# Optimization experiments

Hardware: AMD Instinct MI355X
Metric: run time of the kernel (lower is better)

Reference implementation:

```python
import jax, jax.numpy as jnp
import numpy as np

B, S = 512, 2048
E_DIM, P_DIM, C_DIM, H_DIM = 64, 32, 64, 64
NEG = jnp.float32(-2**32 + 1)  # padding value used by the torch module


def setup_inputs() -> dict:
    key = jax.random.key(0)
    ks = jax.random.split(key, 9)
    return {
        "seq_items": jax.random.normal(ks[0], (B, S, E_DIM), dtype=jnp.float32),
        "seq_pos": jax.random.normal(ks[1], (B, S, P_DIM), dtype=jnp.float32),
        "target_item": jax.random.normal(ks[2], (B, C_DIM), dtype=jnp.float32),
        "Wp": jax.random.normal(ks[3], (P_DIM, H_DIM), dtype=jnp.float32) * (2.0 / (P_DIM + H_DIM)) ** 0.5,
        "We": jax.random.normal(ks[4], (E_DIM, H_DIM), dtype=jnp.float32) * (2.0 / (E_DIM + H_DIM)) ** 0.5,
        "Wc": jax.random.normal(ks[5], (C_DIM, H_DIM), dtype=jnp.float32) * (2.0 / (C_DIM + H_DIM)) ** 0.5,
        "b": jnp.zeros((H_DIM,), dtype=jnp.float32),
        "z": jnp.ones((H_DIM,), dtype=jnp.float32),
        "seq_len": jax.random.randint(ks[6], (B,), 0, S, dtype=jnp.int32),
    }


def reference(seq_items, seq_pos, target_item, Wp, We, Wc, b, z, seq_len):
    # Projections: [B,h] and [B,S,h]
    out_c = target_item @ Wc                      # [B, h]
    out_e = jnp.einsum("bse,eh->bsh", seq_items, We)
    out_p = jnp.einsum("bsp,ph->bsh", seq_pos, Wp)
    # Additive attention score: [B, S]
    a = jnp.sum(jnp.tanh(out_c[:, None, :] + out_p + out_e + b) * z, axis=-1)
    # seq_len mask
    mask = jnp.arange(seq_items.shape[1])[None, :] < seq_len[:, None]  # [B, S]
    score = jax.nn.softmax(jnp.where(mask, a, NEG), axis=1)            # [B, S]
    # u = score @ e -> [B, 1, e_dim]  (intended unsqueeze(1) matmul)
    u = jnp.einsum("bs,bse->be", score, seq_items)[:, None, :]
    # r = sum of masked raw scores -> [B, 1]
    r = jnp.sum(jnp.where(mask, a, 0.0), axis=1, keepdims=True)
    return (u, r)
```

## Files before the change

### kernel.cpp

```cpp
#include <hip/hip_runtime.h>
#include <math.h>

#define B_ 512
#define S_ 2048
#define E_DIM 64
#define P_DIM 32
#define H_DIM 64

typedef short s16x8 __attribute__((ext_vector_type(8)));
typedef float f32x4 __attribute__((ext_vector_type(4)));

__device__ __forceinline__ float wave_reduce_sum(float v) {
#pragma unroll
  for (int m = 32; m >= 1; m >>= 1) v += __shfl_xor(v, m, 64);
  return v;
}

__device__ __forceinline__ float wave_reduce_max(float v) {
#pragma unroll
  for (int m = 32; m >= 1; m >>= 1) v = fmaxf(v, __shfl_xor(v, m, 64));
  return v;
}

__device__ __forceinline__ float tanh_fast(float x) {
  float e = __expf(2.0f * x);
  return 1.0f - 2.0f * __builtin_amdgcn_rcpf(e + 1.0f);
}

__device__ __forceinline__ short bf16b(float x) {
  union { float f; unsigned u; } a;
  a.f = x;
  unsigned r = (a.u + 0x7FFFu + ((a.u >> 16) & 1u)) >> 16;
  return (short)r;
}

__global__ __launch_bounds__(256) void scores_mfma_kernel(
    const float* __restrict__ seq_items, const float* __restrict__ seq_pos,
    const float* __restrict__ target_item, const float* __restrict__ Wp,
    const float* __restrict__ We, const float* __restrict__ Wc,
    const float* __restrict__ bias, const float* __restrict__ z,
    const int* __restrict__ seq_len, float* __restrict__ a_out) {
  const int blk = blockIdx.x;
  const int b = blk >> 4;
  const int s0 = (blk & 15) << 7;
  const int L = seq_len[b];
  if (s0 >= L) return;

  __shared__ s16x8 lds_b[12 * 64];
  __shared__ float c_part[4 * 64];

  const int tid = threadIdx.x;
  const int l = tid & 63;
  const int w = tid >> 6;
  const int cc = l & 15;
  const int q = l >> 4;

#pragma unroll
  for (int i = 0; i < 3; ++i) {
    const int f = w * 3 + i;
    const int kstep = f >> 2;
    const int nt = f & 3;
    const float* __restrict__ src =
        (kstep < 2) ? (We + (size_t)(kstep * 32 + q * 8) * H_DIM + nt * 16 + cc)
                    : (Wp + (size_t)(q * 8) * H_DIM + nt * 16 + cc);
    s16x8 v;
#pragma unroll
    for (int j = 0; j < 8; ++j) v[j] = bf16b(src[(size_t)j * H_DIM]);
    lds_b[f * 64 + l] = v;
  }

  {
    const float* __restrict__ tg = target_item + b * 64;
    float cp = (w == 0) ? bias[l] : 0.0f;
#pragma unroll
    for (int e = 0; e < 16; ++e)
      cp = fmaf(tg[w * 16 + e], Wc[(w * 16 + e) * H_DIM + l], cp);
    c_part[w * 64 + l] = cp;
  }
  __syncthreads();

  s16x8 bfr[12];
#pragma unroll
  for (int f = 0; f < 12; ++f) bfr[f] = lds_b[f * 64 + l];

  float ch[4], zh[4];
#pragma unroll
  for (int nt = 0; nt < 4; ++nt) {
    const int h = nt * 16 + cc;
    ch[nt] = c_part[h] + c_part[64 + h] + c_part[128 + h] + c_part[192 + h];
    zh[nt] = z[h];
  }

  const float* __restrict__ itemsB = seq_items + (size_t)b * S_ * E_DIM;
  const float* __restrict__ posB = seq_pos + (size_t)b * S_ * P_DIM;
  float* __restrict__ aB = a_out + (size_t)b * S_;

#pragma unroll
  for (int mt = 0; mt < 2; ++mt) {
    const int rb = s0 + w * 32 + mt * 16;
    const int s = rb + cc;
    f32x4 acc[4] = {};

#pragma unroll
    for (int kk = 0; kk < 2; ++kk) {
      const float* __restrict__ p = itemsB + (size_t)s * E_DIM + kk * 32 + q * 8;
      const float4 x0 = ((const float4*)p)[0];
      const float4 x1 = ((const float4*)p)[1];
      s16x8 af;
      af[0] = bf16b(x0.x); af[1] = bf16b(x0.y);
      af[2] = bf16b(x0.z); af[3] = bf16b(x0.w);
      af[4] = bf16b(x1.x); af[5] = bf16b(x1.y);
      af[6] = bf16b(x1.z); af[7] = bf16b(x1.w);
#pragma unroll
      for (int nt = 0; nt < 4; ++nt)
        acc[nt] = __builtin_amdgcn_mfma_f32_16x16x32_bf16(af, bfr[kk * 4 + nt],
                                                          acc[nt], 0, 0, 0);
    }
    {
      const float* __restrict__ p = posB + (size_t)s * P_DIM + q * 8;
      const float4 x0 = ((const float4*)p)[0];
      const float4 x1 = ((const float4*)p)[1];
      s16x8 af;
      af[0] = bf16b(x0.x); af[1] = bf16b(x0.y);
      af[2] = bf16b(x0.z); af[3] = bf16b(x0.w);
      af[4] = bf16b(x1.x); af[5] = bf16b(x1.y);
      af[6] = bf16b(x1.z); af[7] = bf16b(x1.w);
#pragma unroll
      for (int nt = 0; nt < 4; ++nt)
        acc[nt] = __builtin_amdgcn_mfma_f32_16x16x32_bf16(af, bfr[8 + nt],
                                                          acc[nt], 0, 0, 0);
    }

    float asum[4];
#pragma unroll
    for (int r = 0; r < 4; ++r) {
      float t = tanh_fast(acc[0][r] + ch[0]) * zh[0];
      t += tanh_fast(acc[1][r] + ch[1]) * zh[1];
      t += tanh_fast(acc[2][r] + ch[2]) * zh[2];
      t += tanh_fast(acc[3][r] + ch[3]) * zh[3];
      asum[r] = t;
    }
#pragma unroll
    for (int r = 0; r < 4; ++r) {
#pragma unroll
      for (int m = 8; m >= 1; m >>= 1) asum[r] += __shfl_xor(asum[r], m, 64);
    }
    if (cc == 0) {
#pragma unroll
      for (int r = 0; r < 4; ++r) aB[rb + q * 4 + r] = asum[r];
    }
  }
}

__global__ __launch_bounds__(256) void softmax_kernel(
    float* __restrict__ a_buf, const int* __restrict__ seq_len,
    float* __restrict__ out) {
  __shared__ float red[4];
  const int b = blockIdx.x;
  const int tid = threadIdx.x;
  const int wv = tid >> 6;
  const int L = seq_len[b];
  float* __restrict__ out_u = out;
  float* __restrict__ out_r = out + B_ * E_DIM;

  if (tid < 64) out_u[b * E_DIM + tid] = 0.0f;

  float* __restrict__ a = a_buf + (size_t)b * S_;

  if (L == 0) {
    const float inv = 1.0f / (float)S_;
    for (int s = tid; s < S_; s += 256) a[s] = inv;
    if (tid == 0) out_r[b] = 0.0f;
    return;
  }

  float av[8];
  float mx = -INFINITY, sa = 0.0f;
#pragma unroll
  for (int i = 0; i < 8; ++i) {
    const int s = tid + 256 * i;
    if (s < L) {
      const float x = a[s];
      av[i] = x;
      mx = fmaxf(mx, x);
      sa += x;
    } else {
      av[i] = 0.0f;
    }
  }
  mx = wave_reduce_max(mx);
  if ((tid & 63) == 0) red[wv] = mx;
  __syncthreads();
  const float m = fmaxf(fmaxf(red[0], red[1]), fmaxf(red[2], red[3]));
  __syncthreads();

  float se = 0.0f;
  float ev[8];
#pragma unroll
  for (int i = 0; i < 8; ++i) {
    const int s = tid + 256 * i;
    if (s < L) {
      const float e = __expf(av[i] - m);
      ev[i] = e;
      se += e;
    } else {
      ev[i] = 0.0f;
    }
  }
  se = wave_reduce_sum(se);
  if ((tid & 63) == 0) red[wv] = se;
  __syncthreads();
  const float l = red[0] + red[1] + red[2] + red[3];
  __syncthreads();
  sa = wave_reduce_sum(sa);
  if ((tid & 63) == 0) red[wv] = sa;
  __syncthreads();
  const float r = red[0] + red[1] + red[2] + red[3];

  const float invl = 1.0f / l;
#pragma unroll
  for (int i = 0; i < 8; ++i) {
    const int s = tid + 256 * i;
    a[s] = (s < L) ? ev[i] * invl : 0.0f;
  }
  if (tid == 0) out_r[b] = r;
}

__global__ __launch_bounds__(256) void wsum_kernel(
    const float* __restrict__ seq_items, const float* __restrict__ w_buf,
    const int* __restrict__ seq_len, float* __restrict__ out) {
  const int blk = blockIdx.x;
  const int b = blk >> 3;
  const int c = blk & 7;
  const int s0 = c << 8;
  const int L = seq_len[b];
  const int Leff = (L == 0) ? S_ : L;
  if (s0 >= Leff) return;
  const int send = min(s0 + 256, Leff);

  const int tid = threadIdx.x;
  const int e4 = tid & 15;
  const int row = tid >> 4;

  const float4* __restrict__ items4 =
      (const float4*)(seq_items + (size_t)b * S_ * E_DIM);
  const float* __restrict__ w = w_buf + (size_t)b * S_;

  float4 acc = make_float4(0.f, 0.f, 0.f, 0.f);
#pragma unroll 4
  for (int s = s0 + row; s < send; s += 16) {
    const float ww = w[s];
    const float4 x = items4[s * 16 + e4];
    acc.x = fmaf(ww, x.x, acc.x);
    acc.y = fmaf(ww, x.y, acc.y);
    acc.z = fmaf(ww, x.z, acc.z);
    acc.w = fmaf(ww, x.w, acc.w);
  }

  __shared__ float4 red[256];
  red[tid] = acc;
  __syncthreads();
  if (tid < 16) {
    float4 sacc = red[tid];
#pragma unroll
    for (int i = 1; i < 16; ++i) {
      const float4 t2 = red[i * 16 + tid];
      sacc.x += t2.x; sacc.y += t2.y; sacc.z += t2.z; sacc.w += t2.w;
    }
    float* dst = out + b * E_DIM + tid * 4;
    atomicAdd(dst + 0, sacc.x);
    atomicAdd(dst + 1, sacc.y);
    atomicAdd(dst + 2, sacc.z);
    atomicAdd(dst + 3, sacc.w);
  }
}

extern "C" void kernel_launch(void* const* d_in, const int* in_sizes, int n_in,
                              void* d_out, int out_size, void* d_ws, size_t ws_size,
                              hipStream_t stream) {
  const float* seq_items = (const float*)d_in[0];
  const float* seq_pos = (const float*)d_in[1];
  const float* target_item = (const float*)d_in[2];
  const float* Wp = (const float*)d_in[3];
  const float* We = (const float*)d_in[4];
  const float* Wc = (const float*)d_in[5];
  const float* bias = (const float*)d_in[6];
  const float* z = (const float*)d_in[7];
  const int* seq_len = (const int*)d_in[8];
  float* out = (float*)d_out;
  float* a_buf = (float*)d_ws;

  scores_mfma_kernel<<<B_ * 16, 256, 0, stream>>>(
      seq_items, seq_pos, target_item, Wp, We, Wc, bias, z, seq_len, a_buf);
  softmax_kernel<<<B_, 256, 0, stream>>>(a_buf, seq_len, out);
  wsum_kernel<<<B_ * 8, 256, 0, stream>>>(seq_items, a_buf, seq_len, out);
}
```

Before: 467.9 us.

## Fuse softmax and weighted sum into score kernel with per-chunk online softmax

Each score block now computes its chunk's local max, exp-sum, raw-score sum and exp-weighted sum of seq_items while the rows are hot. A small combine kernel then merges the per-chunk partials with a rescaled online softmax. This removes the score buffer round trip, the separate softmax pass and the second full read of seq_items. In exchange it adds extra barriers and LDS in the score kernel and relies on cache reuse for the reread rows.

```diff
diff --git a/kernel.cpp b/kernel.cpp
--- a/kernel.cpp
+++ b/kernel.cpp
@@ -6,6 +6,7 @@
 #define E_DIM 64
 #define P_DIM 32
 #define H_DIM 64
+#define CB_STRIDE 68
 
 typedef short s16x8 __attribute__((ext_vector_type(8)));
 typedef float f32x4 __attribute__((ext_vector_type(4)));
@@ -39,15 +40,20 @@
     const float* __restrict__ target_item, const float* __restrict__ Wp,
     const float* __restrict__ We, const float* __restrict__ Wc,
     const float* __restrict__ bias, const float* __restrict__ z,
-    const int* __restrict__ seq_len, float* __restrict__ a_out) {
+    const int* __restrict__ seq_len, float* __restrict__ chunk_buf) {
   const int blk = blockIdx.x;
   const int b = blk >> 4;
   const int s0 = (blk & 15) << 7;
   const int L = seq_len[b];
-  if (s0 >= L) return;
+  const bool uni = (L == 0);
+  if (!uni && s0 >= L) return;
 
   __shared__ s16x8 lds_b[12 * 64];
   __shared__ float c_part[4 * 64];
+  __shared__ float s_a[128];
+  __shared__ float s_w[128];
+  __shared__ __align__(16) float s_pc[4 * 64];
+  __shared__ float redm[4], reds[4], redr[4];
 
   const int tid = threadIdx.x;
   const int l = tid & 63;
@@ -93,7 +99,6 @@
 
   const float* __restrict__ itemsB = seq_items + (size_t)b * S_ * E_DIM;
   const float* __restrict__ posB = seq_pos + (size_t)b * S_ * P_DIM;
-  float* __restrict__ aB = a_out + (size_t)b * S_;
 
 #pragma unroll
   for (int mt = 0; mt < 2; ++mt) {
@@ -147,132 +152,86 @@
     }
     if (cc == 0) {
 #pragma unroll
-      for (int r = 0; r < 4; ++r) aB[rb + q * 4 + r] = asum[r];
-    }
-  }
-}
-
-__global__ __launch_bounds__(256) void softmax_kernel(
-    float* __restrict__ a_buf, const int* __restrict__ seq_len,
+      for (int r = 0; r < 4; ++r) s_a[w * 32 + mt * 16 + q * 4 + r] = asum[r];
+    }
+  }
+
+  __syncthreads();
+  const int row = tid & 127;
+  const int srow = s0 + row;
+  const bool valid = uni || (srow < L);
+  const float araw = s_a[row];
+  const float ae = uni ? 0.0f : araw;
+  float mp = wave_reduce_max(valid ? ae : -INFINITY);
+  if (l == 0) redm[w] = mp;
+  __syncthreads();
+  const float mc = fmaxf(fmaxf(redm[0], redm[1]), fmaxf(redm[2], redm[3]));
+  const float wgt = valid ? __expf(ae - mc) : 0.0f;
+  if (tid < 128) s_w[row] = wgt;
+  const float scp = wave_reduce_sum(wgt);
+  const float rap = wave_reduce_sum(valid ? ae : 0.0f);
+  if (l == 0) { reds[w] = scp; redr[w] = rap; }
+  __syncthreads();
+
+  {
+    const int e4 = l & 15;
+    const int rr = l >> 4;
+    const float4* __restrict__ ip4 =
+        (const float4*)(itemsB + (size_t)(s0 + w * 32) * E_DIM);
+    float4 a4 = make_float4(0.f, 0.f, 0.f, 0.f);
+#pragma unroll
+    for (int i = 0; i < 8; ++i) {
+      const int rloc = rr + i * 4;
+      const float g = s_w[w * 32 + rloc];
+      const float4 x = ip4[rloc * 16 + e4];
+      a4.x = fmaf(g, x.x, a4.x);
+      a4.y = fmaf(g, x.y, a4.y);
+      a4.z = fmaf(g, x.z, a4.z);
+      a4.w = fmaf(g, x.w, a4.w);
+    }
+#pragma unroll
+    for (int m = 16; m <= 32; m <<= 1) {
+      a4.x += __shfl_xor(a4.x, m, 64);
+      a4.y += __shfl_xor(a4.y, m, 64);
+      a4.z += __shfl_xor(a4.z, m, 64);
+      a4.w += __shfl_xor(a4.w, m, 64);
+    }
+    if (rr == 0) *(float4*)&s_pc[w * 64 + e4 * 4] = a4;
+  }
+  __syncthreads();
+
+  float* __restrict__ cb = chunk_buf + (size_t)blk * CB_STRIDE;
+  if (tid < 64) {
+    cb[tid] = s_pc[tid] + s_pc[64 + tid] + s_pc[128 + tid] + s_pc[192 + tid];
+  } else if (tid == 64) {
+    cb[64] = mc;
+  } else if (tid == 65) {
+    cb[65] = reds[0] + reds[1];
+  } else if (tid == 66) {
+    cb[66] = redr[0] + redr[1];
+  }
+}
+
+__global__ __launch_bounds__(64) void combine_kernel(
+    const float* __restrict__ chunk_buf, const int* __restrict__ seq_len,
     float* __restrict__ out) {
-  __shared__ float red[4];
   const int b = blockIdx.x;
-  const int tid = threadIdx.x;
-  const int wv = tid >> 6;
+  const int t = threadIdx.x;
   const int L = seq_len[b];
-  float* __restrict__ out_u = out;
-  float* __restrict__ out_r = out + B_ * E_DIM;
-
-  if (tid < 64) out_u[b * E_DIM + tid] = 0.0f;
-
-  float* __restrict__ a = a_buf + (size_t)b * S_;
-
-  if (L == 0) {
-    const float inv = 1.0f / (float)S_;
-    for (int s = tid; s < S_; s += 256) a[s] = inv;
-    if (tid == 0) out_r[b] = 0.0f;
-    return;
-  }
-
-  float av[8];
-  float mx = -INFINITY, sa = 0.0f;
-#pragma unroll
-  for (int i = 0; i < 8; ++i) {
-    const int s = tid + 256 * i;
-    if (s < L) {
-      const float x = a[s];
-      av[i] = x;
-      mx = fmaxf(mx, x);
-      sa += x;
-    } else {
-      av[i] = 0.0f;
-    }
-  }
-  mx = wave_reduce_max(mx);
-  if ((tid & 63) == 0) red[wv] = mx;
-  __syncthreads();
-  const float m = fmaxf(fmaxf(red[0], red[1]), fmaxf(red[2], red[3]));
-  __syncthreads();
-
-  float se = 0.0f;
-  float ev[8];
-#pragma unroll
-  for (int i = 0; i < 8; ++i) {
-    const int s = tid + 256 * i;
-    if (s < L) {
-      const float e = __expf(av[i] - m);
-      ev[i] = e;
-      se += e;
-    } else {
-      ev[i] = 0.0f;
-    }
-  }
-  se = wave_reduce_sum(se);
-  if ((tid & 63) == 0) red[wv] = se;
-  __syncthreads();
-  const float l = red[0] + red[1] + red[2] + red[3];
-  __syncthreads();
-  sa = wave_reduce_sum(sa);
-  if ((tid & 63) == 0) red[wv] = sa;
-  __syncthreads();
-  const float r = red[0] + red[1] + red[2] + red[3];
-
-  const float invl = 1.0f / l;
-#pragma unroll
-  for (int i = 0; i < 8; ++i) {
-    const int s = tid + 256 * i;
-    a[s] = (s < L) ? ev[i] * invl : 0.0f;
-  }
-  if (tid == 0) out_r[b] = r;
-}
-
-__global__ __launch_bounds__(256) void wsum_kernel(
-    const float* __restrict__ seq_items, const float* __restrict__ w_buf,
-    const int* __restrict__ seq_len, float* __restrict__ out) {
-  const int blk = blockIdx.x;
-  const int b = blk >> 3;
-  const int c = blk & 7;
-  const int s0 = c << 8;
-  const int L = seq_len[b];
-  const int Leff = (L == 0) ? S_ : L;
-  if (s0 >= Leff) return;
-  const int send = min(s0 + 256, Leff);
-
-  const int tid = threadIdx.x;
-  const int e4 = tid & 15;
-  const int row = tid >> 4;
-
-  const float4* __restrict__ items4 =
-      (const float4*)(seq_items + (size_t)b * S_ * E_DIM);
-  const float* __restrict__ w = w_buf + (size_t)b * S_;
-
-  float4 acc = make_float4(0.f, 0.f, 0.f, 0.f);
-#pragma unroll 4
-  for (int s = s0 + row; s < send; s += 16) {
-    const float ww = w[s];
-    const float4 x = items4[s * 16 + e4];
-    acc.x = fmaf(ww, x.x, acc.x);
-    acc.y = fmaf(ww, x.y, acc.y);
-    acc.z = fmaf(ww, x.z, acc.z);
-    acc.w = fmaf(ww, x.w, acc.w);
-  }
-
-  __shared__ float4 red[256];
-  red[tid] = acc;
-  __syncthreads();
-  if (tid < 16) {
-    float4 sacc = red[tid];
-#pragma unroll
-    for (int i = 1; i < 16; ++i) {
-      const float4 t2 = red[i * 16 + tid];
-      sacc.x += t2.x; sacc.y += t2.y; sacc.z += t2.z; sacc.w += t2.w;
-    }
-    float* dst = out + b * E_DIM + tid * 4;
-    atomicAdd(dst + 0, sacc.x);
-    atomicAdd(dst + 1, sacc.y);
-    atomicAdd(dst + 2, sacc.z);
-    atomicAdd(dst + 3, sacc.w);
-  }
+  const int nc = (L == 0) ? 16 : ((L + 127) >> 7);
+  const float* __restrict__ cb = chunk_buf + (size_t)b * 16 * CB_STRIDE;
+
+  float m = -INFINITY;
+  for (int c = 0; c < nc; ++c) m = fmaxf(m, cb[c * CB_STRIDE + 64]);
+  float u = 0.0f, den = 0.0f, r = 0.0f;
+  for (int c = 0; c < nc; ++c) {
+    const float e = __expf(cb[c * CB_STRIDE + 64] - m);
+    u = fmaf(e, cb[c * CB_STRIDE + t], u);
+    den = fmaf(e, cb[c * CB_STRIDE + 65], den);
+    r += cb[c * CB_STRIDE + 66];
+  }
+  out[b * E_DIM + t] = u / den;
+  if (t == 0) out[B_ * E_DIM + b] = r;
 }
 
 extern "C" void kernel_launch(void* const* d_in, const int* in_sizes, int n_in,
@@ -284,14 +243,14 @@
   const float* Wp = (const float*)d_in[3];
   const float* We = (const float*)d_in[4];
   const float* Wc = (const float*)d_in[5];
+  const float* Wc_ = Wc;
   const float* bias = (const float*)d_in[6];
   const float* z = (const float*)d_in[7];
   const int* seq_len = (const int*)d_in[8];
   float* out = (float*)d_out;
-  float* a_buf = (float*)d_ws;
+  float* chunk_buf = (float*)d_ws;
 
   scores_mfma_kernel<<<B_ * 16, 256, 0, stream>>>(
-      seq_items, seq_pos, target_item, Wp, We, Wc, bias, z, seq_len, a_buf);
-  softmax_kernel<<<B_, 256, 0, stream>>>(a_buf, seq_len, out);
-  wsum_kernel<<<B_ * 8, 256, 0, stream>>>(seq_items, a_buf, seq_len, out);
-}
+      seq_items, seq_pos, target_item, Wp, We, Wc_, bias, z, seq_len, chunk_buf);
+  combine_kernel<<<B_, 64, 0, stream>>>(chunk_buf, seq_len, out);
+}
```

New measurement: 458.7 us. Within noise of the previous version (-2.0%).
